# Kernel optimization log

Measured on AMD Instinct MI355X. Metric: run time of the kernel, lower is better.

## Reference

```python
import jax, jax.numpy as jnp
import numpy as np

N = 50000          # nodes
E = 800000         # edges (before self-loops)
IN_CH = 16
HID = 32
HEADS = 4
NEG_SLOPE = 0.2    # PyG GATConv default leaky_relu slope


def add_self_loops(edge_index, n):
    loops = jnp.arange(n, dtype=edge_index.dtype)
    return jnp.concatenate([edge_index, jnp.stack([loops, loops])], axis=1)


def gat_layer(x, edge_index, W, a_src, a_dst, bias, heads, out_ch, concat):
    """PyG-style GATConv: gather -> attention logits -> segment softmax over dst -> scatter."""
    n = x.shape[0]
    h = (x @ W).reshape(n, heads, out_ch)            # [N, H, C]
    src, dst = edge_index[0], edge_index[1]          # messages flow src -> dst
    alpha_src = (h * a_src).sum(-1)                  # [N, H]
    alpha_dst = (h * a_dst).sum(-1)                  # [N, H]
    e = jax.nn.leaky_relu(alpha_src[src] + alpha_dst[dst], NEG_SLOPE)  # [Etot, H]
    # numerically stable segment softmax over incoming edges of each dst node
    e_max = jax.ops.segment_max(e, dst, num_segments=n)
    e_exp = jnp.exp(e - e_max[dst])
    denom = jax.ops.segment_sum(e_exp, dst, num_segments=n)
    alpha = e_exp / (denom[dst] + 1e-16)             # [Etot, H]
    out = jax.ops.segment_sum(h[src] * alpha[..., None], dst, num_segments=n)  # [N, H, C]
    out = out.reshape(n, heads * out_ch) if concat else out.mean(axis=1)
    return out + bias


def setup_inputs() -> dict:
    key = jax.random.key(0)
    ks = jax.random.split(key, 10)
    x = jax.random.normal(ks[0], (N, IN_CH), dtype=jnp.float32)
    edge_index = jax.random.randint(ks[1], (2, E), 0, N, dtype=jnp.int64)
    s = 0.1
    W1 = jax.random.normal(ks[2], (IN_CH, HEADS * HID), dtype=jnp.float32) * s
    a_src1 = jax.random.normal(ks[3], (1, HEADS, HID), dtype=jnp.float32) * s
    a_dst1 = jax.random.normal(ks[4], (1, HEADS, HID), dtype=jnp.float32) * s
    b1 = jnp.zeros((HEADS * HID,), dtype=jnp.float32)
    W2 = jax.random.normal(ks[5], (HEADS * HID, 2), dtype=jnp.float32) * s
    a_src2 = jax.random.normal(ks[6], (1, 1, 2), dtype=jnp.float32) * s
    a_dst2 = jax.random.normal(ks[7], (1, 1, 2), dtype=jnp.float32) * s
    b2 = jnp.zeros((2,), dtype=jnp.float32)
    return {"x": x, "edge_index": edge_index,
            "W1": W1, "a_src1": a_src1, "a_dst1": a_dst1, "b1": b1,
            "W2": W2, "a_src2": a_src2, "a_dst2": a_dst2, "b2": b2}


def reference(x, edge_index, W1, a_src1, a_dst1, b1, W2, a_src2, a_dst2, b2):
    ei = add_self_loops(edge_index, x.shape[0])
    h = gat_layer(x, ei, W1, a_src1, a_dst1, b1, HEADS, HID, concat=True)
    h = jax.nn.relu(h)
    out = gat_layer(h, ei, W2, a_src2, a_dst2, b2, 1, 2, concat=False)
    return out
```

## Files before the change

kernel.cpp:

```cpp
#include <hip/hip_runtime.h>
#include <hip/hip_bf16.h>

#define N_NODES 50000
#define N_EDGES 800000
#define ETOT    (N_EDGES + N_NODES)
#define STRIDE  64
#define IN_CH   16
#define HID     32
#define HEADS   4
#define C1      (HEADS * HID)
#define NEG     0.2f

#define DEG_BLOCKS ((ETOT / 4 + 255) / 256)
#define NGROUPS    (N_NODES / 4)
#define H1_BLOCKS  2048

typedef unsigned short u16;
typedef unsigned int   u32;

__device__ __forceinline__ float bf2f(u16 b) {
    return __uint_as_float(((u32)b) << 16);
}

__device__ __forceinline__ u16 f2bf(float f) {
    __hip_bfloat16 hb = __float2bfloat16(f);
    return *(u16*)&hb;
}

__device__ __forceinline__ int clampn(int v) {
    return v < 0 ? 0 : (v >= N_NODES ? N_NODES - 1 : v);
}

__device__ __forceinline__ int eidx(const int* ei, int e, int i64, int which) {
    int v = i64 ? ei[2 * (which * N_EDGES + e)] : ei[which * N_EDGES + e];
    return clampn(v);
}

__device__ __forceinline__ float cvt(const void* src, int i, int bf) {
    return bf ? bf2f(((const u16*)src)[i]) : ((const float*)src)[i];
}

__device__ __forceinline__ int probe_bf_wave(const u16* xb) {
    int l = threadIdx.x & 63;
    int my = 0;
#pragma unroll
    for (int k = 0; k < 4; k++) {
        float f = bf2f(xb[l * 4 + k]);
        float a = fabsf(f);
        if (f == 0.0f || (a > 9.5e-7f && a < 1.05e6f)) my++;
    }
#pragma unroll
    for (int m = 32; m; m >>= 1) my += __shfl_xor(my, m);
    return my >= 224;
}

__device__ __forceinline__ int probe_i64_wave(const int* ei32) {
    int l = threadIdx.x & 63;
    int nz = (l < 32 && ei32[2 * l + 1] != 0) ? 1 : 0;
#pragma unroll
    for (int m = 32; m; m >>= 1) nz += __shfl_xor(nz, m);
    return nz == 0;
}

__device__ __forceinline__ void dev_degfill(const int* __restrict__ ei,
                                            int* __restrict__ degs,
                                            u16* __restrict__ csr, int blk) {
    int i64 = probe_i64_wave(ei);
    int e0 = (blk * 256 + (int)threadIdx.x) * 4;
    if (e0 >= ETOT) return;
    int s[4], d[4];
#pragma unroll
    for (int j = 0; j < 4; j++) {
        int e = e0 + j;
        if (e < N_EDGES) { s[j] = eidx(ei, e, i64, 0); d[j] = eidx(ei, e, i64, 1); }
        else             { s[j] = d[j] = e - N_EDGES; }
    }
#pragma unroll
    for (int j = 0; j < 4; j++) {
        u32 r = (u32)atomicAdd(&degs[d[j]], 1) + 1u;
        if (r < STRIDE) csr[(size_t)d[j] * STRIDE + r] = (u16)s[j];
    }
}

__device__ __forceinline__ void dev_h1(const void* __restrict__ x,
                                       const void* __restrict__ W1,
                                       const void* __restrict__ a_s,
                                       const void* __restrict__ a_d,
                                       u32* __restrict__ h1u,
                                       float* __restrict__ as1,
                                       float* __restrict__ ad1, int blk) {
    int bf = probe_bf_wave((const u16*)x);
    if (blk == 0 && threadIdx.x < 4) as1[N_NODES * 4 + threadIdx.x] = -1e30f;
    if (blk == 0 && threadIdx.x >= 64 && threadIdx.x < 128)
        h1u[N_NODES * 64 + (threadIdx.x - 64)] = 0;

    int w = threadIdx.x >> 6, l = threadIdx.x & 63;

    float wa[IN_CH], wb[IN_CH];
    if (bf) {
        const u32* w32 = (const u32*)W1;
#pragma unroll
        for (int k = 0; k < IN_CH; k++) {
            u32 v = w32[k * 64 + l];
            wa[k] = bf2f((u16)(v & 0xFFFF));
            wb[k] = bf2f((u16)(v >> 16));
        }
    } else {
        const float2* w64 = (const float2*)W1;
#pragma unroll
        for (int k = 0; k < IN_CH; k++) {
            float2 v = w64[k * 64 + l];
            wa[k] = v.x; wb[k] = v.y;
        }
    }
    float asa, asb, ada, adb;
    if (bf) {
        u32 vs = ((const u32*)a_s)[l], vd = ((const u32*)a_d)[l];
        asa = bf2f((u16)(vs & 0xFFFF)); asb = bf2f((u16)(vs >> 16));
        ada = bf2f((u16)(vd & 0xFFFF)); adb = bf2f((u16)(vd >> 16));
    } else {
        float2 vs = ((const float2*)a_s)[l], vd = ((const float2*)a_d)[l];
        asa = vs.x; asb = vs.y; ada = vd.x; adb = vd.y;
    }

    for (int g = blk; g < NGROUPS; g += H1_BLOCKS) {
        int n = g * 4 + w;
        float xr[IN_CH];
        if (bf) {
            const uint4* xp = (const uint4*)((const u16*)x + (size_t)n * IN_CH);
            uint4 q0 = xp[0], q1 = xp[1];
            u32 qq[8] = {q0.x, q0.y, q0.z, q0.w, q1.x, q1.y, q1.z, q1.w};
#pragma unroll
            for (int k = 0; k < 8; k++) {
                xr[2 * k]     = bf2f((u16)(qq[k] & 0xFFFF));
                xr[2 * k + 1] = bf2f((u16)(qq[k] >> 16));
            }
        } else {
            const float4* xp = (const float4*)((const float*)x + (size_t)n * IN_CH);
#pragma unroll
            for (int k = 0; k < 4; k++) {
                float4 q = xp[k];
                xr[4 * k] = q.x; xr[4 * k + 1] = q.y;
                xr[4 * k + 2] = q.z; xr[4 * k + 3] = q.w;
            }
        }
        float acc0 = 0.f, acc1 = 0.f;
#pragma unroll
        for (int k = 0; k < IN_CH; k++) {
            acc0 += xr[k] * wa[k];
            acc1 += xr[k] * wb[k];
        }
        h1u[n * 64 + l] = (u32)f2bf(acc0) | ((u32)f2bf(acc1) << 16);

        float ps = acc0 * asa + acc1 * asb;
        float pd = acc0 * ada + acc1 * adb;
#pragma unroll
        for (int m = 8; m; m >>= 1) { ps += __shfl_xor(ps, m); pd += __shfl_xor(pd, m); }
        if ((l & 15) == 0) {
            int hd = l >> 4;
            as1[n * 4 + hd] = ps;
            ad1[n * 4 + hd] = pd;
        }
    }
}

__launch_bounds__(256)
__global__ void k_deg_h1(const void* __restrict__ x, const int* __restrict__ ei,
                         const void* __restrict__ W1, const void* __restrict__ a_s,
                         const void* __restrict__ a_d,
                         int* __restrict__ degs, u16* __restrict__ csr,
                         u32* __restrict__ h1u, float* __restrict__ as1,
                         float* __restrict__ ad1) {
    if (blockIdx.x < DEG_BLOCKS) { dev_degfill(ei, degs, csr, blockIdx.x); return; }
    dev_h1(x, W1, a_s, a_d, h1u, as1, ad1, blockIdx.x - DEG_BLOCKS);
}

__launch_bounds__(256)
__global__ void k_gather1(const void* __restrict__ x,
                          const int* __restrict__ degs, const u16* __restrict__ csr,
                          const u32* __restrict__ h1u,
                          const float* __restrict__ as1, const float* __restrict__ ad1,
                          const void* __restrict__ b1, const void* __restrict__ W2,
                          const void* __restrict__ a2s, const void* __restrict__ a2d,
                          float* __restrict__ h2, float* __restrict__ as2,
                          float* __restrict__ ad2) {
    int bf = probe_bf_wave((const u16*)x);
    int n = blockIdx.x * 4 + (threadIdx.x >> 6);
    int l = threadIdx.x & 63;
    int hd = l >> 4;
    int je = l & 7;
    int jh = (l >> 3) & 3;
    float advb = ad1[n * 4 + jh];
    int deg = degs[n] + 1;
    deg = deg > STRIDE ? STRIDE : deg;
    int nb = (deg + 7) >> 3;
    const u16* row = csr + (size_t)n * STRIDE;
    float acc0 = 0.f, acc1 = 0.f, swd = 0.f;

    int se = (int)row[je];
    if (se >= N_NODES) se = N_NODES;
    for (int b = 0; b < nb; b++) {
        int se_next = 0xFFFF;
        if (b + 1 < nb) se_next = (int)row[(b + 1) * 8 + je];
        float t = as1[se * 4 + jh] + advb;
        t = t > 0.f ? t : NEG * t;
        float wm = __expf(t);
        swd += wm;
#pragma unroll
        for (int j = 0; j < 8; j++) {
            int   sj = __shfl(se, j);
            float wj = __shfl(wm, hd * 8 + j);
            u32 p = h1u[sj * 64 + l];
            acc0 += wj * bf2f((u16)(p & 0xFFFF));
            acc1 += wj * bf2f((u16)(p >> 16));
        }
        se = se_next >= N_NODES ? N_NODES : se_next;
    }

    swd += __shfl_xor(swd, 1);
    swd += __shfl_xor(swd, 2);
    swd += __shfl_xor(swd, 4);
    float sw = __shfl(swd, hd * 8);

    float inv = 1.0f / sw;
    float v0 = acc0 * inv + cvt(b1, 2 * l, bf);
    float v1 = acc1 * inv + cvt(b1, 2 * l + 1, bf);
    v0 = v0 > 0.f ? v0 : 0.f;
    v1 = v1 > 0.f ? v1 : 0.f;
    float p0 = v0 * cvt(W2, 4 * l,     bf) + v1 * cvt(W2, 4 * l + 2, bf);
    float p1 = v0 * cvt(W2, 4 * l + 1, bf) + v1 * cvt(W2, 4 * l + 3, bf);
#pragma unroll
    for (int d = 32; d; d >>= 1) { p0 += __shfl_down(p0, d); p1 += __shfl_down(p1, d); }
    if (l == 0) {
        h2[n * 2] = p0; h2[n * 2 + 1] = p1;
        as2[n] = p0 * cvt(a2s, 0, bf) + p1 * cvt(a2s, 1, bf);
        ad2[n] = p0 * cvt(a2d, 0, bf) + p1 * cvt(a2d, 1, bf);
    }
}

__launch_bounds__(256)
__global__ void k_gather2(const void* __restrict__ x,
                          const int* __restrict__ degs, const u16* __restrict__ csr,
                          const float* __restrict__ h2, const float* __restrict__ as2,
                          const float* __restrict__ ad2, const void* __restrict__ b2,
                          void* __restrict__ out) {
    int bf = probe_bf_wave((const u16*)x);
    int n = blockIdx.x * 16 + (threadIdx.x >> 4);
    int g = threadIdx.x & 15;
    float adv = ad2[n], a0 = 0.f, a1 = 0.f, sw = 0.f;
    int deg = degs[n] + 1;
    deg = deg > STRIDE ? STRIDE : deg;
    const u16* row = csr + (size_t)n * STRIDE;
    for (int k = g; k < deg; k += 16) {
        int s = (int)row[k];
        float lg = as2[s] + adv;
        lg = lg > 0.f ? lg : NEG * lg;
        float w = __expf(lg);
        float2 hv = ((const float2*)h2)[s];
        a0 += w * hv.x;
        a1 += w * hv.y;
        sw += w;
    }
#pragma unroll
    for (int m = 8; m; m >>= 1) {
        a0 += __shfl_xor(a0, m); a1 += __shfl_xor(a1, m); sw += __shfl_xor(sw, m);
    }
    if (g == 0) {
        float inv = 1.0f / sw;
        float o0 = a0 * inv + cvt(b2, 0, bf);
        float o1 = a1 * inv + cvt(b2, 1, bf);
        if (bf) {
            ((u32*)out)[n] = (u32)f2bf(o0) | ((u32)f2bf(o1) << 16);
        } else {
            ((float2*)out)[n] = make_float2(o0, o1);
        }
    }
}

extern "C" void kernel_launch(void* const* d_in, const int* in_sizes, int n_in,
                              void* d_out, int out_size, void* d_ws, size_t ws_size,
                              hipStream_t stream) {
    const void* x    = d_in[0];
    const int*  ei   = (const int*)d_in[1];
    const void* W1   = d_in[2];
    const void* a_s1 = d_in[3];
    const void* a_d1 = d_in[4];
    const void* b1   = d_in[5];
    const void* W2   = d_in[6];
    const void* a_s2 = d_in[7];
    const void* a_d2 = d_in[8];
    const void* b2   = d_in[9];

    char* p = (char*)d_ws;
    int*   degs = (int*)p;     p += ((size_t)N_NODES * 4 + 255) & ~255;
    u16*   csr  = (u16*)p;     p += (size_t)N_NODES * STRIDE * 2;
    size_t init_bytes = (size_t)(p - (char*)d_ws);
    u32*   h1u  = (u32*)p;     p += (size_t)(N_NODES + 1) * 64 * 4;
    float* as1  = (float*)p;   p += (size_t)(N_NODES + 1) * HEADS * 4;
    float* ad1  = (float*)p;   p += (size_t)N_NODES * HEADS * 4;
    float* h2   = (float*)p;   p += (size_t)N_NODES * 2 * 4;
    float* as2  = (float*)p;   p += (size_t)N_NODES * 4;
    float* ad2  = (float*)p;   p += (size_t)N_NODES * 4;

    hipMemsetAsync(degs, 0xFF, init_bytes, stream);

    k_deg_h1<<<DEG_BLOCKS + H1_BLOCKS, 256, 0, stream>>>(
        x, ei, W1, a_s1, a_d1, degs, csr, h1u, as1, ad1);
    k_gather1<<<N_NODES / 4, 256, 0, stream>>>(
        x, degs, csr, h1u, as1, ad1, b1, W2, a_s2, a_d2, h2, as2, ad2);
    k_gather2<<<N_NODES / 16, 256, 0, stream>>>(
        x, degs, csr, h2, as2, ad2, b2, d_out);
}
```

Measured before the change: 211.3 us.

## Build CSR via privatized per-copy degree counts and prefix offsets

```diff
diff --git a/kernel.cpp b/kernel.cpp
--- a/kernel.cpp
+++ b/kernel.cpp
@@ -10,6 +10,7 @@
 #define HEADS   4
 #define C1      (HEADS * HID)
 #define NEG     0.2f
+#define NCOPY   8
 
 #define DEG_BLOCKS ((ETOT / 4 + 255) / 256)
 #define NGROUPS    (N_NODES / 4)
@@ -62,23 +63,51 @@
     return nz == 0;
 }
 
-__device__ __forceinline__ void dev_degfill(const int* __restrict__ ei,
-                                            int* __restrict__ degs,
-                                            u16* __restrict__ csr, int blk) {
+__launch_bounds__(256)
+__global__ void k_count(const int* __restrict__ ei, u32* __restrict__ degs8) {
+    int i64 = probe_i64_wave(ei);
+    int blk = blockIdx.x;
+    int e0 = (blk * 256 + (int)threadIdx.x) * 4;
+    if (e0 >= ETOT) return;
+    u32* cnt = degs8 + (size_t)(blk & (NCOPY - 1)) * N_NODES;
+#pragma unroll
+    for (int j = 0; j < 4; j++) {
+        int e = e0 + j;
+        int d = (e < N_EDGES) ? eidx(ei, e, i64, 1) : (e - N_EDGES);
+        atomicAdd(&cnt[d], 1u);
+    }
+}
+
+__launch_bounds__(256)
+__global__ void k_prefix(const u32* __restrict__ degs8, u32* __restrict__ off8,
+                         int* __restrict__ degs) {
+    int n = blockIdx.x * 256 + (int)threadIdx.x;
+    if (n >= N_NODES) return;
+    u32 tot = 0;
+#pragma unroll
+    for (int c = 0; c < NCOPY; c++) {
+        u32 cn = degs8[(size_t)c * N_NODES + n];
+        off8[(size_t)c * N_NODES + n] = (u32)n * STRIDE + tot;
+        tot += cn;
+    }
+    degs[n] = (int)tot;
+}
+
+__device__ __forceinline__ void dev_fill(const int* __restrict__ ei,
+                                         u32* __restrict__ off8,
+                                         u16* __restrict__ csr, int blk) {
     int i64 = probe_i64_wave(ei);
     int e0 = (blk * 256 + (int)threadIdx.x) * 4;
     if (e0 >= ETOT) return;
-    int s[4], d[4];
+    u32* off = off8 + (size_t)(blk & (NCOPY - 1)) * N_NODES;
 #pragma unroll
     for (int j = 0; j < 4; j++) {
         int e = e0 + j;
-        if (e < N_EDGES) { s[j] = eidx(ei, e, i64, 0); d[j] = eidx(ei, e, i64, 1); }
-        else             { s[j] = d[j] = e - N_EDGES; }
-    }
-#pragma unroll
-    for (int j = 0; j < 4; j++) {
-        u32 r = (u32)atomicAdd(&degs[d[j]], 1) + 1u;
-        if (r < STRIDE) csr[(size_t)d[j] * STRIDE + r] = (u16)s[j];
+        int s, d;
+        if (e < N_EDGES) { s = eidx(ei, e, i64, 0); d = eidx(ei, e, i64, 1); }
+        else             { s = d = e - N_EDGES; }
+        u32 slot = atomicAdd(&off[d], 1u);
+        if (slot < (u32)d * STRIDE + STRIDE) csr[slot] = (u16)s;
     }
 }
 
@@ -165,13 +194,13 @@
 }
 
 __launch_bounds__(256)
-__global__ void k_deg_h1(const void* __restrict__ x, const int* __restrict__ ei,
-                         const void* __restrict__ W1, const void* __restrict__ a_s,
-                         const void* __restrict__ a_d,
-                         int* __restrict__ degs, u16* __restrict__ csr,
-                         u32* __restrict__ h1u, float* __restrict__ as1,
-                         float* __restrict__ ad1) {
-    if (blockIdx.x < DEG_BLOCKS) { dev_degfill(ei, degs, csr, blockIdx.x); return; }
+__global__ void k_fill_h1(const void* __restrict__ x, const int* __restrict__ ei,
+                          const void* __restrict__ W1, const void* __restrict__ a_s,
+                          const void* __restrict__ a_d,
+                          u32* __restrict__ off8, u16* __restrict__ csr,
+                          u32* __restrict__ h1u, float* __restrict__ as1,
+                          float* __restrict__ ad1) {
+    if (blockIdx.x < DEG_BLOCKS) { dev_fill(ei, off8, csr, blockIdx.x); return; }
     dev_h1(x, W1, a_s, a_d, h1u, as1, ad1, blockIdx.x - DEG_BLOCKS);
 }
 
@@ -191,7 +220,7 @@
     int je = l & 7;
     int jh = (l >> 3) & 3;
     float advb = ad1[n * 4 + jh];
-    int deg = degs[n] + 1;
+    int deg = degs[n];
     deg = deg > STRIDE ? STRIDE : deg;
     int nb = (deg + 7) >> 3;
     const u16* row = csr + (size_t)n * STRIDE;
@@ -248,7 +277,7 @@
     int n = blockIdx.x * 16 + (threadIdx.x >> 4);
     int g = threadIdx.x & 15;
     float adv = ad2[n], a0 = 0.f, a1 = 0.f, sw = 0.f;
-    int deg = degs[n] + 1;
+    int deg = degs[n];
     deg = deg > STRIDE ? STRIDE : deg;
     const u16* row = csr + (size_t)n * STRIDE;
     for (int k = g; k < deg; k += 16) {
@@ -292,20 +321,24 @@
     const void* b2   = d_in[9];
 
     char* p = (char*)d_ws;
-    int*   degs = (int*)p;     p += ((size_t)N_NODES * 4 + 255) & ~255;
-    u16*   csr  = (u16*)p;     p += (size_t)N_NODES * STRIDE * 2;
-    size_t init_bytes = (size_t)(p - (char*)d_ws);
-    u32*   h1u  = (u32*)p;     p += (size_t)(N_NODES + 1) * 64 * 4;
-    float* as1  = (float*)p;   p += (size_t)(N_NODES + 1) * HEADS * 4;
-    float* ad1  = (float*)p;   p += (size_t)N_NODES * HEADS * 4;
-    float* h2   = (float*)p;   p += (size_t)N_NODES * 2 * 4;
-    float* as2  = (float*)p;   p += (size_t)N_NODES * 4;
-    float* ad2  = (float*)p;   p += (size_t)N_NODES * 4;
-
-    hipMemsetAsync(degs, 0xFF, init_bytes, stream);
-
-    k_deg_h1<<<DEG_BLOCKS + H1_BLOCKS, 256, 0, stream>>>(
-        x, ei, W1, a_s1, a_d1, degs, csr, h1u, as1, ad1);
+    int*   degs  = (int*)p;   p += ((size_t)N_NODES * 4 + 255) & ~255;
+    u32*   degs8 = (u32*)p;   p += (size_t)NCOPY * N_NODES * 4;
+    u32*   off8  = (u32*)p;   p += (size_t)NCOPY * N_NODES * 4;
+    u16*   csr   = (u16*)p;   p += (size_t)N_NODES * STRIDE * 2;
+    u32*   h1u   = (u32*)p;   p += (size_t)(N_NODES + 1) * 64 * 4;
+    float* as1   = (float*)p; p += (size_t)(N_NODES + 1) * HEADS * 4;
+    float* ad1   = (float*)p; p += (size_t)N_NODES * HEADS * 4;
+    float* h2    = (float*)p; p += (size_t)N_NODES * 2 * 4;
+    float* as2   = (float*)p; p += (size_t)N_NODES * 4;
+    float* ad2   = (float*)p; p += (size_t)N_NODES * 4;
+
+    hipMemsetAsync(degs8, 0x00, (size_t)NCOPY * N_NODES * 4, stream);
+    hipMemsetAsync(csr,   0xFF, (size_t)N_NODES * STRIDE * 2, stream);
+
+    k_count<<<DEG_BLOCKS, 256, 0, stream>>>(ei, degs8);
+    k_prefix<<<(N_NODES + 255) / 256, 256, 0, stream>>>(degs8, off8, degs);
+    k_fill_h1<<<DEG_BLOCKS + H1_BLOCKS, 256, 0, stream>>>(
+        x, ei, W1, a_s1, a_d1, off8, csr, h1u, as1, ad1);
     k_gather1<<<N_NODES / 4, 256, 0, stream>>>(
         x, degs, csr, h1u, as1, ad1, b1, W2, a_s2, a_d2, h2, as2, ad2);
     k_gather2<<<N_NODES / 16, 256, 0, stream>>>(
```

Result: slower. 245.3 us (+16.0%).
